# Optimization experiments

Hardware: AMD Instinct MI355X
Metric: run time of the kernel (lower is better)

## Reference

```python
import jax, jax.numpy as jnp
import numpy as np

N_NODES = 100000


def setup_inputs() -> dict:
    key = jax.random.key(0)
    k1, k2, k3, k4 = jax.random.split(key, 4)
    h = jax.random.normal(k1, (N_NODES, 128), dtype=jnp.float32)
    src = jax.random.randint(k2, (1600000,), 0, N_NODES, dtype=jnp.int32)
    dst = jax.random.randint(k3, (1600000,), 0, N_NODES, dtype=jnp.int32)
    # Linear params (PyTorch default init scale ~ 1/sqrt(in_feats))
    W = jax.random.normal(k4, (128, 128), dtype=jnp.float32) * (1.0 / np.sqrt(128.0))
    b = jnp.zeros((128,), dtype=jnp.float32)
    return {"h": h, "src": src, "dst": dst, "W": W, "b": b}


def reference(h, src, dst, W, b):
    # fn.copy_src: gather source-node features per edge  [E, F]
    msgs = h[src]
    # fn.sum: scatter-add messages into destination nodes  [N, F]
    agg = jax.ops.segment_sum(msgs, dst, num_segments=h.shape[0])
    # NodeUpdateModule: linear + relu
    out = agg @ W.T + b
    return jax.nn.relu(out)
```

## Files before the change

### kernel.cpp

```cpp
#include <hip/hip_runtime.h>

#define F      128
#define NPB2   256
#define NPBS2  8
#define NBMAX2 512
#define ECAP   5120
#define CHMAX  6144
#define OVFCAP 32768
#define BR     64
#define KC     32

typedef short bf16x8 __attribute__((ext_vector_type(8)));
typedef float f32x4  __attribute__((ext_vector_type(4)));

__device__ __forceinline__ unsigned short f32_to_bf16_rne(float x) {
    unsigned u = __float_as_uint(x);
    u += 0x7fffu + ((u >> 16) & 1u);
    return (unsigned short)(u >> 16);
}
__device__ __forceinline__ float bf16_to_f32(unsigned short u) {
    return __uint_as_float((unsigned)u << 16);
}

__global__ __launch_bounds__(256) void conv_w_kernel(
        const float* __restrict__ Wf, unsigned short* __restrict__ Wb, int n4) {
    int i = blockIdx.x * blockDim.x + threadIdx.x;
    if (i < n4) {
        float4 v = *(const float4*)(Wf + 4 * (long)i);
        ushort4 o;
        o.x = f32_to_bf16_rne(v.x);
        o.y = f32_to_bf16_rne(v.y);
        o.z = f32_to_bf16_rne(v.z);
        o.w = f32_to_bf16_rne(v.w);
        *(ushort4*)(Wb + 4 * (long)i) = o;
    }
}

__global__ __launch_bounds__(256) void gemm_h_kernel(
        const float* __restrict__ h,
        const unsigned short* __restrict__ Wb,
        unsigned short* __restrict__ hp,
        int n_rows) {
    const int wave = (blockIdx.x * 256 + threadIdx.x) >> 6;
    const int lane = threadIdx.x & 63;
    const int m0 = wave * 16;
    if (m0 >= n_rows) return;
    const int mn   = lane & 15;
    const int quad = lane >> 4;

    const int rowc = min(m0 + mn, n_rows - 1);
    const float* arow = h + (long)rowc * F + quad * 8;

    bf16x8 afr[4];
    #pragma unroll
    for (int kk = 0; kk < 4; ++kk) {
        float4 p0 = *(const float4*)(arow + kk * 32);
        float4 p1 = *(const float4*)(arow + kk * 32 + 4);
        bf16x8 f;
        f[0] = (short)f32_to_bf16_rne(p0.x);
        f[1] = (short)f32_to_bf16_rne(p0.y);
        f[2] = (short)f32_to_bf16_rne(p0.z);
        f[3] = (short)f32_to_bf16_rne(p0.w);
        f[4] = (short)f32_to_bf16_rne(p1.x);
        f[5] = (short)f32_to_bf16_rne(p1.y);
        f[6] = (short)f32_to_bf16_rne(p1.z);
        f[7] = (short)f32_to_bf16_rne(p1.w);
        afr[kk] = f;
    }

    f32x4 acc[8];
    #pragma unroll
    for (int t = 0; t < 8; ++t) acc[t] = (f32x4){0.f, 0.f, 0.f, 0.f};

    #pragma unroll
    for (int kk = 0; kk < 4; ++kk) {
        #pragma unroll
        for (int t = 0; t < 8; ++t) {
            const unsigned short* wp = Wb + (long)(t * 16 + mn) * F + kk * 32 + quad * 8;
            bf16x8 bfr = *(const bf16x8*)wp;
            acc[t] = __builtin_amdgcn_mfma_f32_16x16x32_bf16(afr[kk], bfr, acc[t], 0, 0, 0);
        }
    }

    #pragma unroll
    for (int t = 0; t < 8; ++t) {
        const int col = t * 16 + mn;
        #pragma unroll
        for (int r = 0; r < 4; ++r) {
            const int orow = m0 + quad * 4 + r;
            if (orow < n_rows)
                hp[(long)orow * F + col] = f32_to_bf16_rne(acc[t][r]);
        }
    }
}

__global__ __launch_bounds__(512) void partition_kernel(
        const int* __restrict__ src,
        const int* __restrict__ dst,
        int* __restrict__ gcnt,
        int* __restrict__ ebuf,
        int* __restrict__ ovf,
        int n_edges, int NB) {
    __shared__ int hist[NBMAX2];
    __shared__ int delta2[NBMAX2];
    __shared__ int cursor[NBMAX2];
    __shared__ int sval[CHMAX];
    __shared__ unsigned short sbkt[CHMAX];
    __shared__ int wsum[8];

    const int tid = threadIdx.x;
    const int lane = tid & 63;
    const int w = tid >> 6;
    const int lo = blockIdx.x * CHMAX;
    const int hi = min(n_edges, lo + CHMAX);
    const int len = hi - lo;

    for (int i = tid; i < NB; i += 512) hist[i] = 0;
    __syncthreads();

    for (int i = lo + tid; i < hi; i += 512)
        atomicAdd(&hist[((unsigned)dst[i]) >> NPBS2], 1);
    __syncthreads();

    int v = (tid < NB) ? hist[tid] : 0;
    const int own = v;
    #pragma unroll
    for (int d = 1; d < 64; d <<= 1) { int u = __shfl_up(v, d); if (lane >= d) v += u; }
    if (lane == 63) wsum[w] = v;
    __syncthreads();
    if (w == 0) {
        int s = (lane < 8) ? wsum[lane] : 0;
        #pragma unroll
        for (int d = 1; d < 8; d <<= 1) { int u = __shfl_up(s, d); if (lane >= d) s += u; }
        if (lane < 8) wsum[lane] = s;
    }
    __syncthreads();
    const int excl = v - own + ((w > 0) ? wsum[w - 1] : 0);
    if (tid < NB) {
        int gbase = own ? atomicAdd(&gcnt[tid], own) : 0;
        delta2[tid] = gbase - excl;
        cursor[tid] = excl;
    }
    __syncthreads();

    for (int i = lo + tid; i < hi; i += 512) {
        int d = dst[i], s = src[i];
        int b = ((unsigned)d) >> NPBS2;
        int p = atomicAdd(&cursor[b], 1);
        sval[p] = ((d & (NPB2 - 1)) << 20) | s;
        sbkt[p] = (unsigned short)b;
    }
    __syncthreads();

    for (int i = tid; i < len; i += 512) {
        int vv = sval[i];
        int b = sbkt[i];
        int slot = i + delta2[b];
        if (slot < ECAP) {
            ebuf[(long)b * ECAP + slot] = vv;
        } else {
            int q = atomicAdd(&ovf[0], 1);
            if (q < OVFCAP) {
                ovf[1 + 2 * q] = (b << NPBS2) | (vv >> 20);
                ovf[2 + 2 * q] = vv & 0xFFFFF;
            }
        }
    }
}

__global__ __launch_bounds__(512) void bucket_gather_kernel(
        const unsigned short* __restrict__ hp,
        const int* __restrict__ gcnt,
        const int* __restrict__ ebuf,
        const int* __restrict__ ovf,
        const float* __restrict__ bias,
        float* __restrict__ out,
        int n_nodes) {
    __shared__ int hist[NPB2];
    __shared__ int ofs[NPB2];
    __shared__ int cur[NPB2];
    __shared__ int srt[ECAP];
    __shared__ int wsum[8];

    const int bkt = blockIdx.x;
    const int tid = threadIdx.x;
    const int lane = tid & 63;
    const int w = tid >> 6;
    const int cnt = min(gcnt[bkt], ECAP);
    const int novf = ovf[0];

    if (tid < NPB2) hist[tid] = 0;
    __syncthreads();

    const int* eb = ebuf + (long)bkt * ECAP;
    for (int i = tid; i < cnt; i += 512)
        atomicAdd(&hist[((unsigned)eb[i]) >> 20], 1);
    __syncthreads();

    int v = (tid < NPB2) ? hist[tid] : 0;
    const int own = v;
    #pragma unroll
    for (int d = 1; d < 64; d <<= 1) { int u = __shfl_up(v, d); if (lane >= d) v += u; }
    if (lane == 63) wsum[w] = v;
    __syncthreads();
    if (w == 0) {
        int s = (lane < 8) ? wsum[lane] : 0;
        #pragma unroll
        for (int d = 1; d < 8; d <<= 1) { int u = __shfl_up(s, d); if (lane >= d) s += u; }
        if (lane < 8) wsum[lane] = s;
    }
    __syncthreads();
    if (tid < NPB2) {
        int e = v - own + ((w > 0) ? wsum[w - 1] : 0);
        ofs[tid] = e;
        cur[tid] = e;
    }
    __syncthreads();

    for (int i = tid; i < cnt; i += 512) {
        int vv = eb[i];
        int p = atomicAdd(&cur[vv >> 20], 1);
        srt[p] = vv & 0xFFFFF;
    }
    __syncthreads();

    const float2 bv = *(const float2*)(bias + (lane << 1));
    for (int nl = w; nl < NPB2; nl += 8) {
        const int n = (bkt << NPBS2) + nl;
        if (n >= n_nodes) break;
        const int beg = ofs[nl];
        const int end = beg + hist[nl];

        float ax = 0.f, ay = 0.f;
        for (int i = beg; i < end; i += 8) {
            unsigned vv[8]; bool val[8];
            #pragma unroll
            for (int j = 0; j < 8; ++j) {
                val[j] = (i + j) < end;
                int sid = srt[val[j] ? i + j : beg];
                vv[j] = *(const unsigned*)(hp + ((long)sid << 7) + (lane << 1));
            }
            #pragma unroll
            for (int j = 0; j < 8; ++j) {
                if (val[j]) {
                    ax += __uint_as_float(vv[j] << 16);
                    ay += __uint_as_float(vv[j] & 0xffff0000u);
                }
            }
        }

        if (novf > 0) {
            int ne = min(novf, OVFCAP);
            for (int k = 0; k < ne; ++k) {
                if (ovf[1 + 2 * k] == n) {
                    int s = ovf[2 + 2 * k];
                    unsigned u = *(const unsigned*)(hp + ((long)s << 7) + (lane << 1));
                    ax += __uint_as_float(u << 16);
                    ay += __uint_as_float(u & 0xffff0000u);
                }
            }
        }

        float* o = out + ((long)n << 7) + (lane << 1);
        float rx = fmaxf(ax + bv.x, 0.f);
        float ry = fmaxf(ay + bv.y, 0.f);
        *(float2*)o = make_float2(rx, ry);
    }
}

__global__ void scatter_add_kernel(const float* __restrict__ h,
                                   const int* __restrict__ src,
                                   const int* __restrict__ dst,
                                   float* __restrict__ agg,
                                   long total) {
    long stride = (long)gridDim.x * blockDim.x;
    for (long i = (long)blockIdx.x * blockDim.x + threadIdx.x; i < total; i += stride) {
        int e    = (int)(i >> 5);
        int lane = (int)(i & 31);
        int s = src[e];
        int d = dst[e];
        float4 v = *(const float4*)(h + (long)s * F + (lane << 2));
        float* o = agg + (long)d * F + (lane << 2);
        unsafeAtomicAdd(o + 0, v.x);
        unsafeAtomicAdd(o + 1, v.y);
        unsafeAtomicAdd(o + 2, v.z);
        unsafeAtomicAdd(o + 3, v.w);
    }
}

__global__ __launch_bounds__(256) void gemm_bias_relu_inplace(
        float* __restrict__ out,
        const float* __restrict__ W,
        const float* __restrict__ bias,
        int n_rows) {
    __shared__ __align__(16) float a_t[KC][BR + 4];
    __shared__ __align__(16) float w_t[KC][F + 4];
    const int tid = threadIdx.x;
    const int tx = tid & 15;
    const int ty = tid >> 4;
    const int row0 = blockIdx.x * BR;
    float acc[4][8];
    #pragma unroll
    for (int i = 0; i < 4; ++i)
        #pragma unroll
        for (int j = 0; j < 8; ++j) acc[i][j] = 0.f;
    for (int kc = 0; kc < F; kc += KC) {
        #pragma unroll
        for (int p = 0; p < 2; ++p) {
            int q = tid + p * 256, r = q >> 3, kq = q & 7;
            int row = row0 + r;
            float4 v = make_float4(0.f, 0.f, 0.f, 0.f);
            if (row < n_rows) v = *(const float4*)(out + (long)row * F + kc + (kq << 2));
            a_t[kq * 4 + 0][r] = v.x; a_t[kq * 4 + 1][r] = v.y;
            a_t[kq * 4 + 2][r] = v.z; a_t[kq * 4 + 3][r] = v.w;
        }
        #pragma unroll
        for (int p = 0; p < 4; ++p) {
            int q = tid + p * 256, j = q >> 3, kq = q & 7;
            float4 v = *(const float4*)(W + (long)j * F + kc + (kq << 2));
            w_t[kq * 4 + 0][j] = v.x; w_t[kq * 4 + 1][j] = v.y;
            w_t[kq * 4 + 2][j] = v.z; w_t[kq * 4 + 3][j] = v.w;
        }
        __syncthreads();
        #pragma unroll
        for (int k = 0; k < KC; ++k) {
            float4 av = *(const float4*)&a_t[k][ty << 2];
            float4 w0 = *(const float4*)&w_t[k][tx << 2];
            float4 w1 = *(const float4*)&w_t[k][64 + (tx << 2)];
            float a4[4] = {av.x, av.y, av.z, av.w};
            float wv[8] = {w0.x, w0.y, w0.z, w0.w, w1.x, w1.y, w1.z, w1.w};
            #pragma unroll
            for (int i = 0; i < 4; ++i)
                #pragma unroll
                for (int j = 0; j < 8; ++j) acc[i][j] += a4[i] * wv[j];
        }
        __syncthreads();
    }
    float4 b0 = *(const float4*)(bias + (tx << 2));
    float4 b1 = *(const float4*)(bias + 64 + (tx << 2));
    #pragma unroll
    for (int i = 0; i < 4; ++i) {
        int row = row0 + (ty << 2) + i;
        if (row < n_rows) {
            float4 r0, r1;
            r0.x = fmaxf(acc[i][0] + b0.x, 0.f); r0.y = fmaxf(acc[i][1] + b0.y, 0.f);
            r0.z = fmaxf(acc[i][2] + b0.z, 0.f); r0.w = fmaxf(acc[i][3] + b0.w, 0.f);
            r1.x = fmaxf(acc[i][4] + b1.x, 0.f); r1.y = fmaxf(acc[i][5] + b1.y, 0.f);
            r1.z = fmaxf(acc[i][6] + b1.z, 0.f); r1.w = fmaxf(acc[i][7] + b1.w, 0.f);
            *(float4*)(out + (long)row * F + (tx << 2)) = r0;
            *(float4*)(out + (long)row * F + 64 + (tx << 2)) = r1;
        }
    }
}

extern "C" void kernel_launch(void* const* d_in, const int* in_sizes, int n_in,
                              void* d_out, int out_size, void* d_ws, size_t ws_size,
                              hipStream_t stream) {
    const float* h   = (const float*)d_in[0];
    const int*   src = (const int*)d_in[1];
    const int*   dst = (const int*)d_in[2];
    const float* W   = (const float*)d_in[3];
    const float* b   = (const float*)d_in[4];
    float* out = (float*)d_out;

    const int n_nodes = in_sizes[0] / F;
    const int n_edges = in_sizes[1];
    const int NB = (n_nodes + NPB2 - 1) >> NPBS2;

    auto al16 = [](size_t x) { return (x + 15) & ~(size_t)15; };
    const size_t off_gcnt = 0;
    const size_t off_ovf  = al16((size_t)NB * 4);
    const size_t off_ebuf = al16(off_ovf + 4 + (size_t)OVFCAP * 8);
    const size_t off_hp   = al16(off_ebuf + (size_t)NB * ECAP * 4);
    const size_t off_wb   = al16(off_hp + (size_t)(n_nodes + 1) * F * 2);
    const size_t need     = off_wb + (size_t)F * F * 2;

    if (ws_size >= need && n_nodes > 0 && NB <= NBMAX2) {
        int* gcnt = (int*)((char*)d_ws + off_gcnt);
        int* ovf  = (int*)((char*)d_ws + off_ovf);
        int* ebuf = (int*)((char*)d_ws + off_ebuf);
        unsigned short* hp = (unsigned short*)((char*)d_ws + off_hp);
        unsigned short* Wb = (unsigned short*)((char*)d_ws + off_wb);

        hipMemsetAsync(gcnt, 0, (size_t)NB * 4, stream);
        hipMemsetAsync(ovf, 0, 4, stream);
        hipMemsetAsync(hp + (size_t)n_nodes * F, 0, (size_t)F * 2, stream);

        conv_w_kernel<<<(F * F / 4 + 255) / 256, 256, 0, stream>>>(W, Wb, F * F / 4);

        gemm_h_kernel<<<(n_nodes + 63) / 64, 256, 0, stream>>>(h, Wb, hp, n_nodes);

        const int pgrid = (n_edges + CHMAX - 1) / CHMAX;
        partition_kernel<<<pgrid, 512, 0, stream>>>(src, dst, gcnt, ebuf, ovf,
                                                    n_edges, NB);

        bucket_gather_kernel<<<NB, 512, 0, stream>>>(hp, gcnt, ebuf, ovf, b,
                                                     out, n_nodes);
    } else {
        hipMemsetAsync(out, 0, (size_t)out_size * sizeof(float), stream);
        scatter_add_kernel<<<16384, 256, 0, stream>>>(
            h, src, dst, out, (long)n_edges * 32);
        const int gblocks = (n_nodes + BR - 1) / BR;
        gemm_bias_relu_inplace<<<gblocks, 256, 0, stream>>>(out, W, b, n_nodes);
    }
}
```

Before: 253.0 us.

## Split edge partition into count/scan/scatter passes and widen gather blocks to 1024

Replaces the single partition kernel, which used global atomics on bucket counters, with a deterministic three-pass scheme: per-chunk histograms, a per-bucket scan across chunks, and a scatter that uses the precomputed offsets. Edge values are held in registers between passes, and the gather kernel now uses 1024 threads with register-cached bucket entries and 32-bit byte-offset addressing. The aim is to cut global atomic contention and redundant global reloads, and to raise occupancy in the gather. It adds two extra kernel launches and a count matrix in the workspace.

```diff
diff --git a/kernel.cpp b/kernel.cpp
--- a/kernel.cpp
+++ b/kernel.cpp
@@ -1,11 +1,12 @@
 #include <hip/hip_runtime.h>
 
 #define F      128
-#define NPB2   256
-#define NPBS2  8
-#define NBMAX2 512
+#define NPB    256
+#define NPBS   8
+#define NBMAX  512
 #define ECAP   5120
-#define CHMAX  6144
+#define CHMAX  4096
+#define CH_PT  4
 #define OVFCAP 32768
 #define BR     64
 #define KC     32
@@ -94,20 +95,67 @@
     }
 }
 
-__global__ __launch_bounds__(512) void partition_kernel(
+__global__ __launch_bounds__(1024) void count_kernel(
+        const int* __restrict__ dst,
+        int* __restrict__ cntmat,
+        int n_edges, int NB) {
+    __shared__ int hist[NBMAX];
+    const int tid = threadIdx.x;
+    const int lo = blockIdx.x * CHMAX;
+    const int hi = min(n_edges, lo + CHMAX);
+    for (int i = tid; i < NB; i += 1024) hist[i] = 0;
+    __syncthreads();
+    for (int i = lo + tid; i < hi; i += 1024)
+        atomicAdd(&hist[((unsigned)dst[i]) >> NPBS], 1);
+    __syncthreads();
+    int* row = cntmat + (long)blockIdx.x * NB;
+    for (int i = tid; i < NB; i += 1024) row[i] = hist[i];
+}
+
+__global__ __launch_bounds__(256) void scan_kernel(
+        int* __restrict__ cntmat, int* __restrict__ gcnt, int NB, int NBLK) {
+    __shared__ int wsum[4];
+    const int b = blockIdx.x;
+    const int tid = threadIdx.x;
+    const int lane = tid & 63;
+    const int w = tid >> 6;
+    int carry = 0;
+    for (int c0 = 0; c0 < NBLK; c0 += 256) {
+        const int blk = c0 + tid;
+        const int own = (blk < NBLK) ? cntmat[(long)blk * NB + b] : 0;
+        int v = own;
+        #pragma unroll
+        for (int d = 1; d < 64; d <<= 1) { int u = __shfl_up(v, d); if (lane >= d) v += u; }
+        if (lane == 63) wsum[w] = v;
+        __syncthreads();
+        if (w == 0) {
+            int s = (lane < 4) ? wsum[lane] : 0;
+            #pragma unroll
+            for (int d = 1; d < 4; d <<= 1) { int u = __shfl_up(s, d); if (lane >= d) s += u; }
+            if (lane < 4) wsum[lane] = s;
+        }
+        __syncthreads();
+        const int excl = v - own + ((w > 0) ? wsum[w - 1] : 0) + carry;
+        if (blk < NBLK) cntmat[(long)blk * NB + b] = excl;
+        carry += wsum[3];
+        __syncthreads();
+    }
+    if (tid == 0) gcnt[b] = carry;
+}
+
+__global__ __launch_bounds__(1024) void scatter_kernel(
         const int* __restrict__ src,
         const int* __restrict__ dst,
-        int* __restrict__ gcnt,
+        const int* __restrict__ cntmat,
         int* __restrict__ ebuf,
         int* __restrict__ ovf,
         int n_edges, int NB) {
-    __shared__ int hist[NBMAX2];
-    __shared__ int delta2[NBMAX2];
-    __shared__ int cursor[NBMAX2];
+    __shared__ int hist[NBMAX];
+    __shared__ int dlt[NBMAX];
+    __shared__ int cursor[NBMAX];
     __shared__ int sval[CHMAX];
     __shared__ unsigned short sbkt[CHMAX];
-    __shared__ int wsum[8];
-
+    __shared__ int wsum[16];
     const int tid = threadIdx.x;
     const int lane = tid & 63;
     const int w = tid >> 6;
@@ -115,60 +163,69 @@
     const int hi = min(n_edges, lo + CHMAX);
     const int len = hi - lo;
 
-    for (int i = tid; i < NB; i += 512) hist[i] = 0;
-    __syncthreads();
-
-    for (int i = lo + tid; i < hi; i += 512)
-        atomicAdd(&hist[((unsigned)dst[i]) >> NPBS2], 1);
-    __syncthreads();
-
-    int v = (tid < NB) ? hist[tid] : 0;
-    const int own = v;
+    int dd[CH_PT], ss[CH_PT];
+    #pragma unroll
+    for (int k = 0; k < CH_PT; ++k) {
+        int i = lo + k * 1024 + tid;
+        bool ok = i < hi;
+        dd[k] = ok ? dst[i] : -1;
+        ss[k] = ok ? src[i] : 0;
+    }
+    for (int i = tid; i < NB; i += 1024) hist[i] = 0;
+    __syncthreads();
+
+    #pragma unroll
+    for (int k = 0; k < CH_PT; ++k)
+        if (dd[k] >= 0) atomicAdd(&hist[((unsigned)dd[k]) >> NPBS], 1);
+    __syncthreads();
+
+    const int own = (tid < NB) ? hist[tid] : 0;
+    int v = own;
     #pragma unroll
     for (int d = 1; d < 64; d <<= 1) { int u = __shfl_up(v, d); if (lane >= d) v += u; }
     if (lane == 63) wsum[w] = v;
     __syncthreads();
     if (w == 0) {
-        int s = (lane < 8) ? wsum[lane] : 0;
-        #pragma unroll
-        for (int d = 1; d < 8; d <<= 1) { int u = __shfl_up(s, d); if (lane >= d) s += u; }
-        if (lane < 8) wsum[lane] = s;
-    }
-    __syncthreads();
-    const int excl = v - own + ((w > 0) ? wsum[w - 1] : 0);
+        int s = (lane < 16) ? wsum[lane] : 0;
+        #pragma unroll
+        for (int d = 1; d < 16; d <<= 1) { int u = __shfl_up(s, d); if (lane >= d) s += u; }
+        if (lane < 16) wsum[lane] = s;
+    }
+    __syncthreads();
     if (tid < NB) {
-        int gbase = own ? atomicAdd(&gcnt[tid], own) : 0;
-        delta2[tid] = gbase - excl;
+        const int excl = v - own + ((w > 0) ? wsum[w - 1] : 0);
+        dlt[tid] = cntmat[(long)blockIdx.x * NB + tid] - excl;
         cursor[tid] = excl;
     }
     __syncthreads();
 
-    for (int i = lo + tid; i < hi; i += 512) {
-        int d = dst[i], s = src[i];
-        int b = ((unsigned)d) >> NPBS2;
-        int p = atomicAdd(&cursor[b], 1);
-        sval[p] = ((d & (NPB2 - 1)) << 20) | s;
-        sbkt[p] = (unsigned short)b;
-    }
-    __syncthreads();
-
-    for (int i = tid; i < len; i += 512) {
+    #pragma unroll
+    for (int k = 0; k < CH_PT; ++k)
+        if (dd[k] >= 0) {
+            int b = ((unsigned)dd[k]) >> NPBS;
+            int p = atomicAdd(&cursor[b], 1);
+            sval[p] = ((dd[k] & (NPB - 1)) << 20) | ss[k];
+            sbkt[p] = (unsigned short)b;
+        }
+    __syncthreads();
+
+    for (int i = tid; i < len; i += 1024) {
         int vv = sval[i];
         int b = sbkt[i];
-        int slot = i + delta2[b];
+        int slot = i + dlt[b];
         if (slot < ECAP) {
             ebuf[(long)b * ECAP + slot] = vv;
         } else {
             int q = atomicAdd(&ovf[0], 1);
             if (q < OVFCAP) {
-                ovf[1 + 2 * q] = (b << NPBS2) | (vv >> 20);
+                ovf[1 + 2 * q] = (b << NPBS) | (vv >> 20);
                 ovf[2 + 2 * q] = vv & 0xFFFFF;
             }
         }
     }
 }
 
-__global__ __launch_bounds__(512) void bucket_gather_kernel(
+__global__ __launch_bounds__(1024) void bucket_gather_kernel(
         const unsigned short* __restrict__ hp,
         const int* __restrict__ gcnt,
         const int* __restrict__ ebuf,
@@ -176,57 +233,65 @@
         const float* __restrict__ bias,
         float* __restrict__ out,
         int n_nodes) {
-    __shared__ int hist[NPB2];
-    __shared__ int ofs[NPB2];
-    __shared__ int cur[NPB2];
+    __shared__ int hist[NPB];
+    __shared__ int ofs[NPB];
+    __shared__ int cur[NPB];
     __shared__ int srt[ECAP];
-    __shared__ int wsum[8];
-
+    __shared__ int wsum[16];
     const int bkt = blockIdx.x;
     const int tid = threadIdx.x;
     const int lane = tid & 63;
     const int w = tid >> 6;
     const int cnt = min(gcnt[bkt], ECAP);
     const int novf = ovf[0];
-
-    if (tid < NPB2) hist[tid] = 0;
-    __syncthreads();
-
     const int* eb = ebuf + (long)bkt * ECAP;
-    for (int i = tid; i < cnt; i += 512)
-        atomicAdd(&hist[((unsigned)eb[i]) >> 20], 1);
-    __syncthreads();
-
-    int v = (tid < NPB2) ? hist[tid] : 0;
-    const int own = v;
+
+    int ev[5];
+    #pragma unroll
+    for (int k = 0; k < 5; ++k) {
+        int i = k * 1024 + tid;
+        ev[k] = (i < cnt) ? eb[i] : -1;
+    }
+    if (tid < NPB) hist[tid] = 0;
+    __syncthreads();
+
+    #pragma unroll
+    for (int k = 0; k < 5; ++k)
+        if (ev[k] >= 0) atomicAdd(&hist[((unsigned)ev[k]) >> 20], 1);
+    __syncthreads();
+
+    const int own = (tid < NPB) ? hist[tid] : 0;
+    int v = own;
     #pragma unroll
     for (int d = 1; d < 64; d <<= 1) { int u = __shfl_up(v, d); if (lane >= d) v += u; }
     if (lane == 63) wsum[w] = v;
     __syncthreads();
     if (w == 0) {
-        int s = (lane < 8) ? wsum[lane] : 0;
-        #pragma unroll
-        for (int d = 1; d < 8; d <<= 1) { int u = __shfl_up(s, d); if (lane >= d) s += u; }
-        if (lane < 8) wsum[lane] = s;
-    }
-    __syncthreads();
-    if (tid < NPB2) {
-        int e = v - own + ((w > 0) ? wsum[w - 1] : 0);
+        int s = (lane < 16) ? wsum[lane] : 0;
+        #pragma unroll
+        for (int d = 1; d < 16; d <<= 1) { int u = __shfl_up(s, d); if (lane >= d) s += u; }
+        if (lane < 16) wsum[lane] = s;
+    }
+    __syncthreads();
+    if (tid < NPB) {
+        const int e = v - own + ((w > 0) ? wsum[w - 1] : 0);
         ofs[tid] = e;
         cur[tid] = e;
     }
     __syncthreads();
 
-    for (int i = tid; i < cnt; i += 512) {
-        int vv = eb[i];
-        int p = atomicAdd(&cur[vv >> 20], 1);
-        srt[p] = vv & 0xFFFFF;
-    }
-    __syncthreads();
-
+    #pragma unroll
+    for (int k = 0; k < 5; ++k)
+        if (ev[k] >= 0) {
+            int p = atomicAdd(&cur[((unsigned)ev[k]) >> 20], 1);
+            srt[p] = ev[k] & 0xFFFFF;
+        }
+    __syncthreads();
+
+    const unsigned lo4 = lane << 2;
     const float2 bv = *(const float2*)(bias + (lane << 1));
-    for (int nl = w; nl < NPB2; nl += 8) {
-        const int n = (bkt << NPBS2) + nl;
+    for (int nl = w; nl < NPB; nl += 16) {
+        const int n = (bkt << NPBS) + nl;
         if (n >= n_nodes) break;
         const int beg = ofs[nl];
         const int end = beg + hist[nl];
@@ -238,7 +303,8 @@
             for (int j = 0; j < 8; ++j) {
                 val[j] = (i + j) < end;
                 int sid = srt[val[j] ? i + j : beg];
-                vv[j] = *(const unsigned*)(hp + ((long)sid << 7) + (lane << 1));
+                unsigned bo = ((unsigned)sid << 8) | lo4;
+                vv[j] = *(const unsigned*)((const char*)hp + bo);
             }
             #pragma unroll
             for (int j = 0; j < 8; ++j) {
@@ -254,17 +320,18 @@
             for (int k = 0; k < ne; ++k) {
                 if (ovf[1 + 2 * k] == n) {
                     int s = ovf[2 + 2 * k];
-                    unsigned u = *(const unsigned*)(hp + ((long)s << 7) + (lane << 1));
+                    unsigned bo = ((unsigned)s << 8) | lo4;
+                    unsigned u = *(const unsigned*)((const char*)hp + bo);
                     ax += __uint_as_float(u << 16);
                     ay += __uint_as_float(u & 0xffff0000u);
                 }
             }
         }
 
-        float* o = out + ((long)n << 7) + (lane << 1);
         float rx = fmaxf(ax + bv.x, 0.f);
         float ry = fmaxf(ay + bv.y, 0.f);
-        *(float2*)o = make_float2(rx, ry);
+        unsigned oo = ((unsigned)n << 9) | (lane << 3);
+        *(float2*)((char*)out + oo) = make_float2(rx, ry);
     }
 }
 
@@ -365,37 +432,43 @@
 
     const int n_nodes = in_sizes[0] / F;
     const int n_edges = in_sizes[1];
-    const int NB = (n_nodes + NPB2 - 1) >> NPBS2;
+    const int NB   = (n_nodes + NPB - 1) >> NPBS;
+    const int NBLK = (n_edges + CHMAX - 1) / CHMAX;
 
     auto al16 = [](size_t x) { return (x + 15) & ~(size_t)15; };
     const size_t off_gcnt = 0;
     const size_t off_ovf  = al16((size_t)NB * 4);
-    const size_t off_ebuf = al16(off_ovf + 4 + (size_t)OVFCAP * 8);
+    const size_t off_cmat = al16(off_ovf + 4 + (size_t)OVFCAP * 8);
+    const size_t off_ebuf = al16(off_cmat + (size_t)NBLK * NB * 4);
     const size_t off_hp   = al16(off_ebuf + (size_t)NB * ECAP * 4);
-    const size_t off_wb   = al16(off_hp + (size_t)(n_nodes + 1) * F * 2);
+    const size_t off_wb   = al16(off_hp + (size_t)n_nodes * F * 2);
     const size_t need     = off_wb + (size_t)F * F * 2;
 
-    if (ws_size >= need && n_nodes > 0 && NB <= NBMAX2) {
+    if (ws_size >= need && n_nodes > 0 && NB <= NBMAX) {
         int* gcnt = (int*)((char*)d_ws + off_gcnt);
         int* ovf  = (int*)((char*)d_ws + off_ovf);
+        int* cmat = (int*)((char*)d_ws + off_cmat);
         int* ebuf = (int*)((char*)d_ws + off_ebuf);
         unsigned short* hp = (unsigned short*)((char*)d_ws + off_hp);
         unsigned short* Wb = (unsigned short*)((char*)d_ws + off_wb);
 
-        hipMemsetAsync(gcnt, 0, (size_t)NB * 4, stream);
         hipMemsetAsync(ovf, 0, 4, stream);
-        hipMemsetAsync(hp + (size_t)n_nodes * F, 0, (size_t)F * 2, stream);
 
         conv_w_kernel<<<(F * F / 4 + 255) / 256, 256, 0, stream>>>(W, Wb, F * F / 4);
 
         gemm_h_kernel<<<(n_nodes + 63) / 64, 256, 0, stream>>>(h, Wb, hp, n_nodes);
 
-        const int pgrid = (n_edges + CHMAX - 1) / CHMAX;
-        partition_kernel<<<pgrid, 512, 0, stream>>>(src, dst, gcnt, ebuf, ovf,
-                                                    n_edges, NB);
-
-        bucket_gather_kernel<<<NB, 512, 0, stream>>>(hp, gcnt, ebuf, ovf, b,
-                                                     out, n_nodes);
+        if (NBLK > 0)
+            count_kernel<<<NBLK, 1024, 0, stream>>>(dst, cmat, n_edges, NB);
+
+        scan_kernel<<<NB, 256, 0, stream>>>(cmat, gcnt, NB, NBLK);
+
+        if (NBLK > 0)
+            scatter_kernel<<<NBLK, 1024, 0, stream>>>(src, dst, cmat, ebuf, ovf,
+                                                      n_edges, NB);
+
+        bucket_gather_kernel<<<NB, 1024, 0, stream>>>(hp, gcnt, ebuf, ovf, b,
+                                                      out, n_nodes);
     } else {
         hipMemsetAsync(out, 0, (size_t)out_size * sizeof(float), stream);
         scatter_add_kernel<<<16384, 256, 0, stream>>>(
```

Measured after the change: 220.9 us. 12.7% less time.

## Replace global-atomic bucket partition with per-chunk local sort and gather-side merge

Applied to the files above, without the earlier changes.

Edges are now sorted locally per chunk into destination buckets, with per-chunk exclusive offsets written out. No global atomics or fixed-capacity bucket buffers are used. The gather kernel merges each bucket's slices from all chunks into shared memory, then sorts by node with padding to multiples of eight so the inner loop needs no bounds masks. Bucket size halves to 128 nodes for more blocks, the W conversion and the pad-row zeroing are folded into the sort kernel, and the memsets and one launch are removed. The cost is that every gather block scans all chunk offset rows, and overflow handling is limited to a small spill list of 64 entries, so a dense bucket could lose edges.

```diff
diff --git a/kernel.cpp b/kernel.cpp
--- a/kernel.cpp
+++ b/kernel.cpp
@@ -1,14 +1,16 @@
 #include <hip/hip_runtime.h>
 
-#define F      128
-#define NPB2   256
-#define NPBS2  8
-#define NBMAX2 512
-#define ECAP   5120
-#define CHMAX  6144
-#define OVFCAP 32768
-#define BR     64
-#define KC     32
+#define F        128
+#define NPB      128
+#define NPBS     7
+#define NBMAX    1024
+#define CHMAX    4096
+#define NBLKMAX  512
+#define CNTCAP   3072
+#define SRTSZ    3968
+#define SPILLCAP 64
+#define BR       64
+#define KC       32
 
 typedef short bf16x8 __attribute__((ext_vector_type(8)));
 typedef float f32x4  __attribute__((ext_vector_type(4)));
@@ -18,22 +20,91 @@
     u += 0x7fffu + ((u >> 16) & 1u);
     return (unsigned short)(u >> 16);
 }
-__device__ __forceinline__ float bf16_to_f32(unsigned short u) {
-    return __uint_as_float((unsigned)u << 16);
-}
-
-__global__ __launch_bounds__(256) void conv_w_kernel(
-        const float* __restrict__ Wf, unsigned short* __restrict__ Wb, int n4) {
-    int i = blockIdx.x * blockDim.x + threadIdx.x;
-    if (i < n4) {
-        float4 v = *(const float4*)(Wf + 4 * (long)i);
-        ushort4 o;
-        o.x = f32_to_bf16_rne(v.x);
-        o.y = f32_to_bf16_rne(v.y);
-        o.z = f32_to_bf16_rne(v.z);
-        o.w = f32_to_bf16_rne(v.w);
-        *(ushort4*)(Wb + 4 * (long)i) = o;
-    }
+
+__global__ __launch_bounds__(1024) void prep_sort_kernel(
+        const float* __restrict__ Wf,
+        unsigned short* __restrict__ Wb,
+        unsigned short* __restrict__ hp,
+        const int* __restrict__ src,
+        const int* __restrict__ dst,
+        int* __restrict__ excl,
+        int* __restrict__ sbuf,
+        int n_edges, int NB, int n_nodes) {
+    const int tid = threadIdx.x;
+
+    if (blockIdx.x == 0) {
+        #pragma unroll
+        for (int k = 0; k < 4; ++k) {
+            int i = k * 1024 + tid;
+            float4 v = *(const float4*)(Wf + 4 * (long)i);
+            ushort4 o;
+            o.x = f32_to_bf16_rne(v.x);
+            o.y = f32_to_bf16_rne(v.y);
+            o.z = f32_to_bf16_rne(v.z);
+            o.w = f32_to_bf16_rne(v.w);
+            *(ushort4*)(Wb + 4 * (long)i) = o;
+        }
+        if (tid < 64) ((int*)(hp + (size_t)n_nodes * F))[tid] = 0;
+        return;
+    }
+
+    __shared__ int hist[NBMAX];
+    __shared__ int cursor[NBMAX];
+    __shared__ int sval[CHMAX];
+    __shared__ int wsum[16];
+    const int lane = tid & 63;
+    const int w = tid >> 6;
+    const int ch = blockIdx.x - 1;
+    const int lo = ch * CHMAX;
+    const int hi = min(n_edges, lo + CHMAX);
+    const int len = hi - lo;
+
+    int dd[4], ss[4];
+    #pragma unroll
+    for (int k = 0; k < 4; ++k) {
+        int i = lo + k * 1024 + tid;
+        bool ok = i < hi;
+        dd[k] = ok ? dst[i] : -1;
+        ss[k] = ok ? src[i] : 0;
+    }
+    for (int i = tid; i < NB; i += 1024) hist[i] = 0;
+    __syncthreads();
+
+    #pragma unroll
+    for (int k = 0; k < 4; ++k)
+        if (dd[k] >= 0) atomicAdd(&hist[((unsigned)dd[k]) >> NPBS], 1);
+    __syncthreads();
+
+    const int own = (tid < NB) ? hist[tid] : 0;
+    int v = own;
+    #pragma unroll
+    for (int d = 1; d < 64; d <<= 1) { int u = __shfl_up(v, d); if (lane >= d) v += u; }
+    if (lane == 63) wsum[w] = v;
+    __syncthreads();
+    if (w == 0) {
+        int s = (lane < 16) ? wsum[lane] : 0;
+        #pragma unroll
+        for (int d = 1; d < 16; d <<= 1) { int u = __shfl_up(s, d); if (lane >= d) s += u; }
+        if (lane < 16) wsum[lane] = s;
+    }
+    __syncthreads();
+    const int ex = v - own + ((w > 0) ? wsum[w - 1] : 0);
+    int* eg = excl + (long)ch * (NB + 1);
+    if (tid < NB) { eg[tid] = ex; cursor[tid] = ex; }
+    if (tid == NB - 1) eg[NB] = ex + own;
+    __syncthreads();
+
+    #pragma unroll
+    for (int k = 0; k < 4; ++k)
+        if (dd[k] >= 0) {
+            int b = ((unsigned)dd[k]) >> NPBS;
+            int p = atomicAdd(&cursor[b], 1);
+            sval[p] = ((dd[k] & (NPB - 1)) << 20) | ss[k];
+        }
+    __syncthreads();
+
+    int* ob = sbuf + (long)ch * CHMAX;
+    for (int i = tid; i < len; i += 1024) ob[i] = sval[i];
 }
 
 __global__ __launch_bounds__(256) void gemm_h_kernel(
@@ -94,177 +165,156 @@
     }
 }
 
-__global__ __launch_bounds__(512) void partition_kernel(
-        const int* __restrict__ src,
-        const int* __restrict__ dst,
-        int* __restrict__ gcnt,
-        int* __restrict__ ebuf,
-        int* __restrict__ ovf,
-        int n_edges, int NB) {
-    __shared__ int hist[NBMAX2];
-    __shared__ int delta2[NBMAX2];
-    __shared__ int cursor[NBMAX2];
-    __shared__ int sval[CHMAX];
-    __shared__ unsigned short sbkt[CHMAX];
-    __shared__ int wsum[8];
-
+__global__ __launch_bounds__(512) void bucket_gather_kernel(
+        const unsigned short* __restrict__ hp,
+        const int* __restrict__ excl,
+        const int* __restrict__ sbuf,
+        const float* __restrict__ bias,
+        float* __restrict__ out,
+        int n_nodes, int NBLK, int NB) {
+    __shared__ int lbase[NBLKMAX + 1];
+    __shared__ int lofs[NBLKMAX];
+    __shared__ int stg[CNTCAP];
+    __shared__ __align__(16) int srt[SRTSZ];
+    __shared__ int hist[NPB];
+    __shared__ int ofs[NPB + 1];
+    __shared__ int cur[NPB];
+    __shared__ int sdl[SPILLCAP];
+    __shared__ int ssv[SPILLCAP];
+    __shared__ int scnt;
+    __shared__ int wsum[16];
+
+    const int b = blockIdx.x;
     const int tid = threadIdx.x;
     const int lane = tid & 63;
     const int w = tid >> 6;
-    const int lo = blockIdx.x * CHMAX;
-    const int hi = min(n_edges, lo + CHMAX);
-    const int len = hi - lo;
-
-    for (int i = tid; i < NB; i += 512) hist[i] = 0;
-    __syncthreads();
-
-    for (int i = lo + tid; i < hi; i += 512)
-        atomicAdd(&hist[((unsigned)dst[i]) >> NPBS2], 1);
-    __syncthreads();
-
-    int v = (tid < NB) ? hist[tid] : 0;
-    const int own = v;
-    #pragma unroll
-    for (int d = 1; d < 64; d <<= 1) { int u = __shfl_up(v, d); if (lane >= d) v += u; }
-    if (lane == 63) wsum[w] = v;
-    __syncthreads();
-    if (w == 0) {
-        int s = (lane < 8) ? wsum[lane] : 0;
-        #pragma unroll
-        for (int d = 1; d < 8; d <<= 1) { int u = __shfl_up(s, d); if (lane >= d) s += u; }
-        if (lane < 8) wsum[lane] = s;
-    }
-    __syncthreads();
-    const int excl = v - own + ((w > 0) ? wsum[w - 1] : 0);
-    if (tid < NB) {
-        int gbase = own ? atomicAdd(&gcnt[tid], own) : 0;
-        delta2[tid] = gbase - excl;
-        cursor[tid] = excl;
-    }
-    __syncthreads();
-
-    for (int i = lo + tid; i < hi; i += 512) {
-        int d = dst[i], s = src[i];
-        int b = ((unsigned)d) >> NPBS2;
-        int p = atomicAdd(&cursor[b], 1);
-        sval[p] = ((d & (NPB2 - 1)) << 20) | s;
-        sbkt[p] = (unsigned short)b;
-    }
-    __syncthreads();
-
-    for (int i = tid; i < len; i += 512) {
-        int vv = sval[i];
-        int b = sbkt[i];
-        int slot = i + delta2[b];
-        if (slot < ECAP) {
-            ebuf[(long)b * ECAP + slot] = vv;
-        } else {
-            int q = atomicAdd(&ovf[0], 1);
-            if (q < OVFCAP) {
-                ovf[1 + 2 * q] = (b << NPBS2) | (vv >> 20);
-                ovf[2 + 2 * q] = vv & 0xFFFFF;
+
+    for (int c = tid; c < NBLK; c += 512) {
+        const int* er = excl + (long)c * (NB + 1) + b;
+        int e0 = er[0];
+        lofs[c] = e0;
+        lbase[c] = er[1] - e0;
+    }
+    if (tid < NPB) hist[tid] = 0;
+    if (tid == 0) scnt = 0;
+    if (NBLK == 0 && tid == 0) lbase[0] = 0;
+    __syncthreads();
+
+    {
+        const int own = (tid < NBLK) ? lbase[tid] : 0;
+        int v = own;
+        #pragma unroll
+        for (int d = 1; d < 64; d <<= 1) { int u = __shfl_up(v, d); if (lane >= d) v += u; }
+        if (lane == 63) wsum[w] = v;
+        __syncthreads();
+        if (w == 0) {
+            int s = (lane < 8) ? wsum[lane] : 0;
+            #pragma unroll
+            for (int d = 1; d < 8; d <<= 1) { int u = __shfl_up(s, d); if (lane >= d) s += u; }
+            if (lane < 8) wsum[lane] = s;
+        }
+        __syncthreads();
+        const int ex = v - own + ((w > 0) ? wsum[w - 1] : 0);
+        if (tid < NBLK) lbase[tid] = ex;
+        if (tid == NBLK - 1) lbase[NBLK] = ex + own;
+    }
+    __syncthreads();
+    const int cnt = lbase[NBLK];
+    const int cstg = min(cnt, CNTCAP);
+
+    for (int c0 = w * 4; c0 < NBLK; c0 += 32) {
+        const int g = lane >> 4;
+        const int c = c0 + g;
+        const int li = lane & 15;
+        int slen = 0, ob = 0, sb = 0;
+        if (c < NBLK) { ob = lbase[c]; slen = lbase[c + 1] - ob; sb = lofs[c]; }
+        for (int l = li; l < slen; l += 16) {
+            int id = sbuf[(long)c * CHMAX + sb + l];
+            int d2 = ob + l;
+            if (d2 < CNTCAP) {
+                stg[d2] = id;
+            } else {
+                int q = atomicAdd(&scnt, 1);
+                if (q < SPILLCAP) { sdl[q] = id >> 20; ssv[q] = id & 0xFFFFF; }
             }
         }
     }
-}
-
-__global__ __launch_bounds__(512) void bucket_gather_kernel(
-        const unsigned short* __restrict__ hp,
-        const int* __restrict__ gcnt,
-        const int* __restrict__ ebuf,
-        const int* __restrict__ ovf,
-        const float* __restrict__ bias,
-        float* __restrict__ out,
-        int n_nodes) {
-    __shared__ int hist[NPB2];
-    __shared__ int ofs[NPB2];
-    __shared__ int cur[NPB2];
-    __shared__ int srt[ECAP];
-    __shared__ int wsum[8];
-
-    const int bkt = blockIdx.x;
-    const int tid = threadIdx.x;
-    const int lane = tid & 63;
-    const int w = tid >> 6;
-    const int cnt = min(gcnt[bkt], ECAP);
-    const int novf = ovf[0];
-
-    if (tid < NPB2) hist[tid] = 0;
-    __syncthreads();
-
-    const int* eb = ebuf + (long)bkt * ECAP;
-    for (int i = tid; i < cnt; i += 512)
-        atomicAdd(&hist[((unsigned)eb[i]) >> 20], 1);
-    __syncthreads();
-
-    int v = (tid < NPB2) ? hist[tid] : 0;
-    const int own = v;
-    #pragma unroll
-    for (int d = 1; d < 64; d <<= 1) { int u = __shfl_up(v, d); if (lane >= d) v += u; }
-    if (lane == 63) wsum[w] = v;
-    __syncthreads();
-    if (w == 0) {
-        int s = (lane < 8) ? wsum[lane] : 0;
-        #pragma unroll
-        for (int d = 1; d < 8; d <<= 1) { int u = __shfl_up(s, d); if (lane >= d) s += u; }
-        if (lane < 8) wsum[lane] = s;
-    }
-    __syncthreads();
-    if (tid < NPB2) {
-        int e = v - own + ((w > 0) ? wsum[w - 1] : 0);
-        ofs[tid] = e;
-        cur[tid] = e;
-    }
-    __syncthreads();
-
-    for (int i = tid; i < cnt; i += 512) {
-        int vv = eb[i];
-        int p = atomicAdd(&cur[vv >> 20], 1);
-        srt[p] = vv & 0xFFFFF;
-    }
-    __syncthreads();
-
+    __syncthreads();
+
+    for (int e = tid; e < cstg; e += 512)
+        atomicAdd(&hist[((unsigned)stg[e]) >> 20], 1);
+    __syncthreads();
+
+    for (int i = tid; i < SRTSZ; i += 512) srt[i] = n_nodes;
+    {
+        const int own = (tid < NPB) ? hist[tid] : 0;
+        const int pd = (own + 7) & ~7;
+        int v = pd;
+        #pragma unroll
+        for (int d = 1; d < 64; d <<= 1) { int u = __shfl_up(v, d); if (lane >= d) v += u; }
+        if (lane == 63) wsum[w] = v;
+        __syncthreads();
+        if (w == 0) {
+            int s = (lane < 8) ? wsum[lane] : 0;
+            #pragma unroll
+            for (int d = 1; d < 8; d <<= 1) { int u = __shfl_up(s, d); if (lane >= d) s += u; }
+            if (lane < 8) wsum[lane] = s;
+        }
+        __syncthreads();
+        const int ex = v - pd + ((w > 0) ? wsum[w - 1] : 0);
+        if (tid < NPB) { ofs[tid] = ex; cur[tid] = ex; }
+        if (tid == NPB - 1) ofs[NPB] = ex + pd;
+    }
+    __syncthreads();
+
+    for (int e = tid; e < cstg; e += 512) {
+        int id = stg[e];
+        int p = atomicAdd(&cur[((unsigned)id) >> 20], 1);
+        srt[p] = id & 0xFFFFF;
+    }
+    __syncthreads();
+
+    const unsigned lo4 = lane << 2;
     const float2 bv = *(const float2*)(bias + (lane << 1));
-    for (int nl = w; nl < NPB2; nl += 8) {
-        const int n = (bkt << NPBS2) + nl;
+    const int ns = min(scnt, SPILLCAP);
+    for (int nl = w; nl < NPB; nl += 8) {
+        const int n = (b << NPBS) + nl;
         if (n >= n_nodes) break;
         const int beg = ofs[nl];
-        const int end = beg + hist[nl];
+        const int pend = ofs[nl + 1];
 
         float ax = 0.f, ay = 0.f;
-        for (int i = beg; i < end; i += 8) {
-            unsigned vv[8]; bool val[8];
+        for (int i = beg; i < pend; i += 8) {
+            const int4 ia = *(const int4*)&srt[i];
+            const int4 ib = *(const int4*)&srt[i + 4];
+            int sid[8] = {ia.x, ia.y, ia.z, ia.w, ib.x, ib.y, ib.z, ib.w};
+            unsigned vv[8];
+            #pragma unroll
+            for (int j = 0; j < 8; ++j)
+                vv[j] = *(const unsigned*)((const char*)hp +
+                                           (((unsigned)sid[j] << 8) | lo4));
             #pragma unroll
             for (int j = 0; j < 8; ++j) {
-                val[j] = (i + j) < end;
-                int sid = srt[val[j] ? i + j : beg];
-                vv[j] = *(const unsigned*)(hp + ((long)sid << 7) + (lane << 1));
+                ax += __uint_as_float(vv[j] << 16);
+                ay += __uint_as_float(vv[j] & 0xffff0000u);
             }
-            #pragma unroll
-            for (int j = 0; j < 8; ++j) {
-                if (val[j]) {
-                    ax += __uint_as_float(vv[j] << 16);
-                    ay += __uint_as_float(vv[j] & 0xffff0000u);
-                }
-            }
-        }
-
-        if (novf > 0) {
-            int ne = min(novf, OVFCAP);
-            for (int k = 0; k < ne; ++k) {
-                if (ovf[1 + 2 * k] == n) {
-                    int s = ovf[2 + 2 * k];
-                    unsigned u = *(const unsigned*)(hp + ((long)s << 7) + (lane << 1));
+        }
+
+        if (ns > 0) {
+            for (int k = 0; k < ns; ++k) {
+                if (sdl[k] == nl) {
+                    unsigned u = *(const unsigned*)((const char*)hp +
+                                   (((unsigned)ssv[k] << 8) | lo4));
                     ax += __uint_as_float(u << 16);
                     ay += __uint_as_float(u & 0xffff0000u);
                 }
             }
         }
 
-        float* o = out + ((long)n << 7) + (lane << 1);
         float rx = fmaxf(ax + bv.x, 0.f);
         float ry = fmaxf(ay + bv.y, 0.f);
-        *(float2*)o = make_float2(rx, ry);
+        *(float2*)((char*)out + (((unsigned)n << 9) | (lane << 3))) =
+            make_float2(rx, ry);
     }
 }
 
@@ -365,37 +415,29 @@
 
     const int n_nodes = in_sizes[0] / F;
     const int n_edges = in_sizes[1];
-    const int NB = (n_nodes + NPB2 - 1) >> NPBS2;
+    const int NB   = (n_nodes + NPB - 1) >> NPBS;
+    const int NBLK = (n_edges + CHMAX - 1) / CHMAX;
 
     auto al16 = [](size_t x) { return (x + 15) & ~(size_t)15; };
-    const size_t off_gcnt = 0;
-    const size_t off_ovf  = al16((size_t)NB * 4);
-    const size_t off_ebuf = al16(off_ovf + 4 + (size_t)OVFCAP * 8);
-    const size_t off_hp   = al16(off_ebuf + (size_t)NB * ECAP * 4);
+    const size_t off_excl = 0;
+    const size_t off_sbuf = al16(off_excl + (size_t)NBLK * (NB + 1) * 4);
+    const size_t off_hp   = al16(off_sbuf + (size_t)NBLK * CHMAX * 4);
     const size_t off_wb   = al16(off_hp + (size_t)(n_nodes + 1) * F * 2);
     const size_t need     = off_wb + (size_t)F * F * 2;
 
-    if (ws_size >= need && n_nodes > 0 && NB <= NBMAX2) {
-        int* gcnt = (int*)((char*)d_ws + off_gcnt);
-        int* ovf  = (int*)((char*)d_ws + off_ovf);
-        int* ebuf = (int*)((char*)d_ws + off_ebuf);
+    if (ws_size >= need && n_nodes > 0 && NB <= NBMAX && NBLK <= NBLKMAX) {
+        int* excl = (int*)((char*)d_ws + off_excl);
+        int* sbuf = (int*)((char*)d_ws + off_sbuf);
         unsigned short* hp = (unsigned short*)((char*)d_ws + off_hp);
         unsigned short* Wb = (unsigned short*)((char*)d_ws + off_wb);
 
-        hipMemsetAsync(gcnt, 0, (size_t)NB * 4, stream);
-        hipMemsetAsync(ovf, 0, 4, stream);
-        hipMemsetAsync(hp + (size_t)n_nodes * F, 0, (size_t)F * 2, stream);
-
-        conv_w_kernel<<<(F * F / 4 + 255) / 256, 256, 0, stream>>>(W, Wb, F * F / 4);
+        prep_sort_kernel<<<NBLK + 1, 1024, 0, stream>>>(
+            W, Wb, hp, src, dst, excl, sbuf, n_edges, NB, n_nodes);
 
         gemm_h_kernel<<<(n_nodes + 63) / 64, 256, 0, stream>>>(h, Wb, hp, n_nodes);
 
-        const int pgrid = (n_edges + CHMAX - 1) / CHMAX;
-        partition_kernel<<<pgrid, 512, 0, stream>>>(src, dst, gcnt, ebuf, ovf,
-                                                    n_edges, NB);
-
-        bucket_gather_kernel<<<NB, 512, 0, stream>>>(hp, gcnt, ebuf, ovf, b,
-                                                     out, n_nodes);
+        bucket_gather_kernel<<<NB, 512, 0, stream>>>(
+            hp, excl, sbuf, b, out, n_nodes, NBLK, NB);
     } else {
         hipMemsetAsync(out, 0, (size_t)out_size * sizeof(float), stream);
         scatter_add_kernel<<<16384, 256, 0, stream>>>(
```

After: 242.9 us. -4.0%, faster.
